# Optimization experiments

Hardware: AMD Instinct MI355X
Metric: run time of the kernel (lower is better)

## Reference

```python
import jax, jax.numpy as jnp
import numpy as np

B, N, L = 32, 1024, 128
K, D_E, H = 3, 16, 4


def setup_inputs() -> dict:
    key = jax.random.key(0)
    ks = jax.random.split(key, 7)
    return {
        "x": jax.random.normal(ks[0], (B, N, L), jnp.float32),
        # mild scaling on embeddings/projections keeps softmax logits in a sane range
        "psi_emb": jax.random.normal(ks[1], (N, D_E), jnp.float32) * 0.3,
        "psi": jnp.float32(1.0),
        "W_q": jax.random.normal(ks[2], (D_E, H, D_E), jnp.float32) * 0.2,
        "W_k": jax.random.normal(ks[3], (D_E, H, D_E), jnp.float32) * 0.2,
        "attn_alpha": jnp.float32(0.5),
        "F_w": jax.random.normal(ks[4], (H, D_E, K + 1, L), jnp.float32) * 0.1,
        "f_b": jax.random.normal(ks[5], (H, D_E), jnp.float32),
        "head_mix": jnp.ones((H,), jnp.float32),
    }


def reference(x, psi_emb, psi, W_q, W_k, attn_alpha, F_w, f_b, head_mix):
    # x: (B, N, L)
    n = x.shape[1]
    # --- gaussian adjacency: softmax over columns of exp(-psi * ||psi_i - psi_j||^2)
    diff = psi_emb[:, None, :] - psi_emb[None, :, :]          # (N, N, d_e)
    dist2 = jnp.sum(diff * diff, axis=-1)                     # (N, N)
    A_base = jax.nn.softmax(jnp.exp(-psi * dist2), axis=1)    # (N, N)
    # --- per-head attention adjacency
    Q = jnp.einsum('nd,dhm->nhm', psi_emb, W_q)               # (N, H, d_e)
    Kt = jnp.einsum('nd,dhm->nhm', psi_emb, W_k)              # (N, H, d_e)
    scale = 1.0 / jnp.sqrt(jnp.asarray(Q.shape[-1], x.dtype))
    A_attn = jax.nn.softmax(
        jnp.einsum('nhd,mhd->hnm', Q, Kt) * scale, axis=-1)   # (H, N, N)
    # --- sigmoid blend (all heads at once)
    alpha = jax.nn.sigmoid(attn_alpha)
    A_eff = alpha * A_base[None] + (1.0 - alpha) * A_attn     # (H, N, N)
    # --- Chebyshev recursion: T0 = I, T1 = A, Tk = 2 A T_{k-1} - T_{k-2}
    I = jnp.broadcast_to(jnp.eye(n, dtype=x.dtype), A_eff.shape)
    supports = [I, A_eff]
    for _ in range(2, K + 1):
        supports.append(2.0 * jnp.einsum('hnm,hml->hnl', A_eff, supports[-1]) - supports[-2])
    S = jnp.stack(supports, axis=1)                           # (H, K+1, N, N)
    # --- per-node filters
    W_filter = jnp.einsum('nd,hdkl->hnkl', psi_emb, F_w)      # (H, N, K+1, L)
    b_filter = jnp.einsum('nd,hd->hn', psi_emb, f_b)          # (H, N)
    # --- graph conv + node-specific contraction
    x_g = jnp.einsum('hknm,bml->bhknl', S, x)                 # (B, H, K+1, N, L)
    out_h = jnp.einsum('bhknl,hnkl->bhn', x_g, W_filter) + b_filter[None]
    # --- head mixing
    mix_w = jax.nn.softmax(head_mix, axis=0)                  # (H,)
    return jnp.einsum('bhn,h->bn', out_h, mix_w)              # (B, N)
```

## Files before the change

### kernel.cpp

```cpp
#include <hip/hip_runtime.h>
#include <cstdint>

#define NN 1024
#define BB 32
#define LL 128
#define DE 16
#define HH 4
#define K1 4
#define BD 512
#define NS 524288

using bf16x8 = __attribute__((ext_vector_type(8))) short;
using f32x4  = __attribute__((ext_vector_type(4))) float;

__device__ inline unsigned short f2bf(float f) {
    unsigned u = __builtin_bit_cast(unsigned, f);
    u += 0x7FFFu + ((u >> 16) & 1u);
    return (unsigned short)(u >> 16);
}
__device__ inline float bf2f(unsigned short u) {
    return __builtin_bit_cast(float, (unsigned)u << 16);
}

struct LogitsSmem {
    float ejs[64][17];
    float eis[64][17];
    float kjs[64][64];
    float qis[4][64][17];
    float part[4][5][64];
    float wq[1024];
    float wk[1024];
};
struct XtSmem { float xs[64][128]; };

__global__ __launch_bounds__(256) void phase1(
    const float* __restrict__ psi_emb, const float* __restrict__ psi_p,
    const float* __restrict__ W_q, const float* __restrict__ W_k,
    const float* __restrict__ x, const float* __restrict__ F_w,
    short* __restrict__ bnt, short* __restrict__ ant, float* __restrict__ partials,
    short* __restrict__ xt, short* __restrict__ wtt, float* __restrict__ out)
{
    __shared__ __align__(16) char smem_raw[sizeof(LogitsSmem)];
    const int bid = blockIdx.x;
    const int tid = threadIdx.x;

    if (bid < 256) {
        LogitsSmem& S = *(LogitsSmem*)smem_raw;
        const int jb = bid & 15, ib = bid >> 4;
        const int i0 = ib * 64, j0 = jb * 64;
        {
            const int row = tid >> 2, dq = (tid & 3) * 4;
            const float4 vj = *(const float4*)(psi_emb + (j0 + row) * DE + dq);
            S.ejs[row][dq] = vj.x; S.ejs[row][dq + 1] = vj.y;
            S.ejs[row][dq + 2] = vj.z; S.ejs[row][dq + 3] = vj.w;
            const float4 vi = *(const float4*)(psi_emb + (i0 + row) * DE + dq);
            S.eis[row][dq] = vi.x; S.eis[row][dq + 1] = vi.y;
            S.eis[row][dq + 2] = vi.z; S.eis[row][dq + 3] = vi.w;
            *(float4*)&S.wq[tid * 4] = *(const float4*)(W_q + tid * 4);
            *(float4*)&S.wk[tid * 4] = *(const float4*)(W_k + tid * 4);
        }
        __syncthreads();
#pragma unroll
        for (int rep = 0; rep < 16; rep++) {
            const int idx = rep * 256 + tid;
            const int row = idx >> 6, hm = idx & 63;
            float qv = 0.f, kv = 0.f;
#pragma unroll
            for (int d = 0; d < DE; d++) {
                qv += S.eis[row][d] * S.wq[d * 64 + hm];
                kv += S.ejs[row][d] * S.wk[d * 64 + hm];
            }
            S.qis[hm >> 4][row][hm & 15] = qv;
            S.kjs[row][hm] = kv;
        }
        __syncthreads();

        const int i = tid & 63, jg = tid >> 6;
        const float psi = psi_p[0];
        float er[DE];
#pragma unroll
        for (int d = 0; d < DE; d++) er[d] = S.eis[i][d];

        float sb = 0.f, sa[HH] = {0.f, 0.f, 0.f, 0.f};
#pragma unroll
        for (int g = 0; g < 2; g++) {
            unsigned short bw[8];
#pragma unroll
            for (int r = 0; r < 8; r++) {
                const int j = jg * 16 + g * 8 + r;
                float d2 = 0.f;
#pragma unroll
                for (int d = 0; d < DE; d++) { const float t = er[d] - S.ejs[j][d]; d2 += t * t; }
                const float bn = __expf(__expf(-psi * d2));
                sb += bn;
                bw[r] = f2bf(bn);
            }
            uint4 pk;
            pk.x = bw[0] | ((unsigned)bw[1] << 16);
            pk.y = bw[2] | ((unsigned)bw[3] << 16);
            pk.z = bw[4] | ((unsigned)bw[5] << 16);
            pk.w = bw[6] | ((unsigned)bw[7] << 16);
            const size_t toff = (size_t)((j0 + jg * 16 + g * 8) >> 3) * 8192 + (size_t)(i0 + i) * 8;
            *(uint4*)(bnt + toff) = pk;
        }
#pragma unroll
        for (int h = 0; h < HH; h++) {
            float qr[DE];
#pragma unroll
            for (int m = 0; m < DE; m++) qr[m] = S.qis[h][i][m];
#pragma unroll
            for (int g = 0; g < 2; g++) {
                unsigned short aw[8];
#pragma unroll
                for (int r = 0; r < 8; r++) {
                    const int j = jg * 16 + g * 8 + r;
                    float dot = 0.f;
#pragma unroll
                    for (int m = 0; m < DE; m++) dot += qr[m] * S.kjs[j][h * DE + m];
                    const float an = __expf(dot * 0.25f);
                    sa[h] += an;
                    aw[r] = f2bf(an);
                }
                uint4 pk;
                pk.x = aw[0] | ((unsigned)aw[1] << 16);
                pk.y = aw[2] | ((unsigned)aw[3] << 16);
                pk.z = aw[4] | ((unsigned)aw[5] << 16);
                pk.w = aw[6] | ((unsigned)aw[7] << 16);
                const size_t toff = (size_t)((j0 + jg * 16 + g * 8) >> 3) * 8192 + (size_t)(i0 + i) * 8;
                *(uint4*)(ant + (size_t)h * 1048576 + toff) = pk;
            }
        }
        S.part[jg][0][i] = sb;
#pragma unroll
        for (int h = 0; h < HH; h++) S.part[jg][1 + h][i] = sa[h];
        __syncthreads();
        if (tid < 64) {
#pragma unroll
            for (int s = 0; s < 5; s++) {
                const float v = S.part[0][s][tid] + S.part[1][s][tid] +
                                S.part[2][s][tid] + S.part[3][s][tid];
                partials[(size_t)jb * 5120 + (size_t)s * 1024 + i0 + tid] = v;
            }
        }
    } else if (bid < 768) {
        XtSmem& X = *(XtSmem*)smem_raw;
        const int idx = bid - 256;
        const int m0 = (idx & 15) * 64;
        const int b  = idx >> 4;
        for (int i = tid; i < 2048; i += 256) {
            const int row = i >> 5, lq = i & 31;
            *(float4*)&X.xs[row][lq * 4] =
                *(const float4*)(x + ((size_t)(b * NN + m0 + row)) * LL + lq * 4);
        }
        __syncthreads();
        for (int j = tid; j < 1024; j += 256) {
            const int m = j & 63, lc = j >> 6;
            const float* s = &X.xs[m][lc * 8];
            uint4 pk;
            pk.x = f2bf(s[0]) | ((unsigned)f2bf(s[1]) << 16);
            pk.y = f2bf(s[2]) | ((unsigned)f2bf(s[3]) << 16);
            pk.z = f2bf(s[4]) | ((unsigned)f2bf(s[5]) << 16);
            pk.w = f2bf(s[6]) | ((unsigned)f2bf(s[7]) << 16);
            *(uint4*)(xt + (size_t)b * 131072 + (size_t)lc * 8192 + (size_t)(m0 + m) * 8) = pk;
        }
    } else if (bid < 784) {
        const int j = (bid - 768) * 256 + tid;
        const int lc = j >> 8, c = j & 255;
        const int h = c >> 6, k = (c >> 4) & 3, d = c & 15;
        const float* s = F_w + (size_t)((h * DE + d) * K1 + k) * LL + lc * 8;
        uint4 pk;
        pk.x = f2bf(s[0]) | ((unsigned)f2bf(s[1]) << 16);
        pk.y = f2bf(s[2]) | ((unsigned)f2bf(s[3]) << 16);
        pk.z = f2bf(s[4]) | ((unsigned)f2bf(s[5]) << 16);
        pk.w = f2bf(s[6]) | ((unsigned)f2bf(s[7]) << 16);
        *(uint4*)(wtt + (size_t)lc * 2048 + (size_t)c * 8) = pk;
    } else {
        const int idx = (bid - 784) * 256 + tid;
        const float4 z = {0.f, 0.f, 0.f, 0.f};
        *(float4*)(out + (size_t)idx * 8) = z;
        *(float4*)(out + (size_t)idx * 8 + 4) = z;
    }
}

__global__ __launch_bounds__(256) void phase2(
    const short* __restrict__ xt, const short* __restrict__ wtt,
    short* __restrict__ Gt,
    const short* __restrict__ bnt, const short* __restrict__ ant,
    const float* __restrict__ partials, const float* __restrict__ alpha_p,
    short* __restrict__ At)
{
    const int bid = blockIdx.x;
    const int tid = threadIdx.x;
    __shared__ float sums_l[5][64];

    if (bid < 1024) {
        const int cb = bid & 3;
        const int m0 = ((bid >> 2) & 15) * 64;
        const int bp = bid >> 6;
        const int wave = tid >> 6, lane = tid & 63;
        const int b  = bp * 2 + (wave >> 1);
        const int wc = wave & 1;
        const int q = lane >> 4, m16 = lane & 15;
        const short* xb = xt + (size_t)b * 131072;

        f32x4 acc[4][2];
#pragma unroll
        for (int mi = 0; mi < 4; mi++)
#pragma unroll
            for (int ni = 0; ni < 2; ni++) acc[mi][ni] = (f32x4){0.f, 0.f, 0.f, 0.f};

#pragma unroll
        for (int ks = 0; ks < 4; ks++) {
            const int kc = ks * 4 + q;
            bf16x8 a[4], bb[2];
#pragma unroll
            for (int mi = 0; mi < 4; mi++)
                a[mi] = *(const bf16x8*)(xb + (size_t)kc * 8192 + (size_t)(m0 + mi * 16 + m16) * 8);
#pragma unroll
            for (int ni = 0; ni < 2; ni++)
                bb[ni] = *(const bf16x8*)(wtt + (size_t)kc * 2048 +
                                          (size_t)(cb * 64 + wc * 32 + ni * 16 + m16) * 8);
#pragma unroll
            for (int mi = 0; mi < 4; mi++)
#pragma unroll
                for (int ni = 0; ni < 2; ni++)
                    acc[mi][ni] = __builtin_amdgcn_mfma_f32_16x16x32_bf16(a[mi], bb[ni], acc[mi][ni], 0, 0, 0);
        }

#pragma unroll
        for (int ni = 0; ni < 2; ni++) {
            const int cc = cb * 64 + wc * 32 + ni * 16 + m16;
            const int kk = (cc >> 4) & 3, hh = cc >> 6;
            const int col512 = b * 16 + (cc & 15);
            short* gdst = Gt + (size_t)(kk * 4 + hh) * 524288;
#pragma unroll
            for (int mi = 0; mi < 4; mi++) {
                const int row0 = m0 + mi * 16 + q * 4;
                ushort4 pk;
                pk.x = f2bf(acc[mi][ni][0]); pk.y = f2bf(acc[mi][ni][1]);
                pk.z = f2bf(acc[mi][ni][2]); pk.w = f2bf(acc[mi][ni][3]);
                *(ushort4*)(gdst + ((size_t)(row0 >> 3) * 512 + col512) * 8 + (row0 & 7)) = pk;
            }
        }
    } else {
        const int idx = bid - 1024;
        const int jb = idx & 15, ib = idx >> 4;
        const int i0 = ib * 64, j0 = jb * 64;
        const int lane = tid & 63, w = tid >> 6;
        {
            float acc = 0.f;
#pragma unroll
            for (int jb2 = 0; jb2 < 16; jb2++)
                acc += partials[(size_t)jb2 * 5120 + (size_t)w * 1024 + i0 + lane];
            sums_l[w][lane] = acc;
            if (w == 0) {
                float a4 = 0.f;
#pragma unroll
                for (int jb2 = 0; jb2 < 16; jb2++)
                    a4 += partials[(size_t)jb2 * 5120 + 4 * 1024 + i0 + lane];
                sums_l[4][lane] = a4;
            }
        }
        __syncthreads();
        const int i = lane, jg = w;
        const float alpha = 1.f / (1.f + __expf(-alpha_p[0]));
        const float ibs = alpha / sums_l[0][i];
        float ias[HH];
#pragma unroll
        for (int h = 0; h < HH; h++) ias[h] = (1.f - alpha) / sums_l[1 + h][i];

#pragma unroll
        for (int g = 0; g < 2; g++) {
            const size_t toff = (size_t)((j0 + jg * 16 + g * 8) >> 3) * 8192 + (size_t)(i0 + i) * 8;
            const uint4 bp = *(const uint4*)(bnt + toff);
            float bnv[8];
            bnv[0] = bf2f(bp.x & 0xFFFF); bnv[1] = bf2f(bp.x >> 16);
            bnv[2] = bf2f(bp.y & 0xFFFF); bnv[3] = bf2f(bp.y >> 16);
            bnv[4] = bf2f(bp.z & 0xFFFF); bnv[5] = bf2f(bp.z >> 16);
            bnv[6] = bf2f(bp.w & 0xFFFF); bnv[7] = bf2f(bp.w >> 16);
#pragma unroll
            for (int h = 0; h < HH; h++) {
                const uint4 ap = *(const uint4*)(ant + (size_t)h * 1048576 + toff);
                float av[8];
                av[0] = bf2f(ap.x & 0xFFFF); av[1] = bf2f(ap.x >> 16);
                av[2] = bf2f(ap.y & 0xFFFF); av[3] = bf2f(ap.y >> 16);
                av[4] = bf2f(ap.z & 0xFFFF); av[5] = bf2f(ap.z >> 16);
                av[6] = bf2f(ap.w & 0xFFFF); av[7] = bf2f(ap.w >> 16);
                unsigned short ow[8];
#pragma unroll
                for (int r = 0; r < 8; r++) ow[r] = f2bf(ibs * bnv[r] + ias[h] * av[r]);
                uint4 pk;
                pk.x = ow[0] | ((unsigned)ow[1] << 16);
                pk.y = ow[2] | ((unsigned)ow[3] << 16);
                pk.z = ow[4] | ((unsigned)ow[5] << 16);
                pk.w = ow[6] | ((unsigned)ow[7] << 16);
                *(uint4*)(At + (size_t)h * 1048576 + toff) = pk;
            }
        }
    }
}

__global__ __launch_bounds__(256) void gemm_mf(
    const short* __restrict__ At, const short* __restrict__ Bt,
    const short* __restrict__ Pt, const short* __restrict__ Qt,
    short* __restrict__ Ot, float scale, float pc, float qc)
{
    const int h = blockIdx.z;
    const short* Ah = At + (size_t)h * 1048576;
    const short* Bh = Bt + (size_t)h * 524288;
    const short* Ph = Pt + (size_t)h * 524288;
    const short* Qh = Qt + (size_t)h * 524288;
    short* Oh = Ot + (size_t)h * 524288;

    const int c0 = blockIdx.x * 64;
    const int r0 = blockIdx.y * 64;
    const int tid = threadIdx.x;
    const int wave = tid >> 6, lane = tid & 63;
    const int q = lane >> 4, m16 = lane & 15;
    const int wr = wave >> 1, wc = wave & 1;

    __shared__ __align__(16) short As[2][2048];
    __shared__ __align__(16) short Bs[2][2048];

    {
        uint4 ra = *(const uint4*)(Ah + ((size_t)wave * 1024 + r0 + lane) * 8);
        uint4 rb = *(const uint4*)(Bh + ((size_t)wave * 512 + c0 + lane) * 8);
        *(uint4*)&As[0][wave * 512 + lane * 8] = ra;
        *(uint4*)&Bs[0][wave * 512 + lane * 8] = rb;
    }
    __syncthreads();

    f32x4 acc[2][2];
#pragma unroll
    for (int mi = 0; mi < 2; mi++)
#pragma unroll
        for (int ni = 0; ni < 2; ni++) acc[mi][ni] = (f32x4){0.f, 0.f, 0.f, 0.f};

    int buf = 0;
    for (int k0 = 32; k0 <= 1024; k0 += 32) {
        uint4 na, nb;
        const bool more = (k0 < 1024);
        if (more) {
            na = *(const uint4*)(Ah + (((size_t)(k0 >> 3) + wave) * 1024 + r0 + lane) * 8);
            nb = *(const uint4*)(Bh + (((size_t)(k0 >> 3) + wave) * 512 + c0 + lane) * 8);
        }
        bf16x8 af0 = *(const bf16x8*)&As[buf][q * 512 + (wr * 32 + m16) * 8];
        bf16x8 af1 = *(const bf16x8*)&As[buf][q * 512 + (wr * 32 + 16 + m16) * 8];
        bf16x8 bf0 = *(const bf16x8*)&Bs[buf][q * 512 + (wc * 32 + m16) * 8];
        bf16x8 bf1 = *(const bf16x8*)&Bs[buf][q * 512 + (wc * 32 + 16 + m16) * 8];
        acc[0][0] = __builtin_amdgcn_mfma_f32_16x16x32_bf16(af0, bf0, acc[0][0], 0, 0, 0);
        acc[0][1] = __builtin_amdgcn_mfma_f32_16x16x32_bf16(af0, bf1, acc[0][1], 0, 0, 0);
        acc[1][0] = __builtin_amdgcn_mfma_f32_16x16x32_bf16(af1, bf0, acc[1][0], 0, 0, 0);
        acc[1][1] = __builtin_amdgcn_mfma_f32_16x16x32_bf16(af1, bf1, acc[1][1], 0, 0, 0);
        if (more) {
            const int nx = buf ^ 1;
            *(uint4*)&As[nx][wave * 512 + lane * 8] = na;
            *(uint4*)&Bs[nx][wave * 512 + lane * 8] = nb;
            __syncthreads();
            buf = nx;
        }
    }

#pragma unroll
    for (int mi = 0; mi < 2; mi++) {
        const int row0 = r0 + wr * 32 + mi * 16 + q * 4;
#pragma unroll
        for (int ni = 0; ni < 2; ni++) {
            const int cc = c0 + wc * 32 + ni * 16 + m16;
            const size_t off = ((size_t)(row0 >> 3) * 512 + cc) * 8 + (row0 & 7);
            const ushort4 pv = *(const ushort4*)(Ph + off);
            float v[4];
            v[0] = scale * acc[mi][ni][0] + pc * bf2f(pv.x);
            v[1] = scale * acc[mi][ni][1] + pc * bf2f(pv.y);
            v[2] = scale * acc[mi][ni][2] + pc * bf2f(pv.z);
            v[3] = scale * acc[mi][ni][3] + pc * bf2f(pv.w);
            if (qc != 0.f) {
                const ushort4 qv = *(const ushort4*)(Qh + off);
                v[0] += qc * bf2f(qv.x); v[1] += qc * bf2f(qv.y);
                v[2] += qc * bf2f(qv.z); v[3] += qc * bf2f(qv.w);
            }
            ushort4 pk;
            pk.x = f2bf(v[0]); pk.y = f2bf(v[1]); pk.z = f2bf(v[2]); pk.w = f2bf(v[3]);
            *(ushort4*)(Oh + off) = pk;
        }
    }
}

__global__ __launch_bounds__(256) void gemm3_out(
    const short* __restrict__ At, const short* __restrict__ Bt,
    const short* __restrict__ Pt, const short* __restrict__ Qt,
    const float* __restrict__ psi_emb, const float* __restrict__ f_b,
    const float* __restrict__ head_mix, float* __restrict__ out)
{
    const int h = blockIdx.z;
    const short* Ah = At + (size_t)h * 1048576;
    const short* Bh = Bt + (size_t)h * 524288;
    const short* Ph = Pt + (size_t)h * 524288;
    const short* Qh = Qt + (size_t)h * 524288;

    const int c0 = blockIdx.x * 64;
    const int r0 = blockIdx.y * 64;
    const int tid = threadIdx.x;
    const int wave = tid >> 6, lane = tid & 63;
    const int q = lane >> 4, m16 = lane & 15;
    const int wr = wave >> 1, wc = wave & 1;

    __shared__ __align__(16) short As[2][2048];
    __shared__ __align__(16) short Bs[2][2048];
    __shared__ float es[64][17];

    {
        uint4 ra = *(const uint4*)(Ah + ((size_t)wave * 1024 + r0 + lane) * 8);
        uint4 rb = *(const uint4*)(Bh + ((size_t)wave * 512 + c0 + lane) * 8);
        *(uint4*)&As[0][wave * 512 + lane * 8] = ra;
        *(uint4*)&Bs[0][wave * 512 + lane * 8] = rb;
        const int row = tid >> 2, dq = (tid & 3) * 4;
        const float4 ev = *(const float4*)(psi_emb + (size_t)(r0 + row) * DE + dq);
        es[row][dq] = ev.x; es[row][dq + 1] = ev.y;
        es[row][dq + 2] = ev.z; es[row][dq + 3] = ev.w;
    }
    __syncthreads();

    f32x4 acc[2][2];
#pragma unroll
    for (int mi = 0; mi < 2; mi++)
#pragma unroll
        for (int ni = 0; ni < 2; ni++) acc[mi][ni] = (f32x4){0.f, 0.f, 0.f, 0.f};

    int buf = 0;
    for (int k0 = 32; k0 <= 1024; k0 += 32) {
        uint4 na, nb;
        const bool more = (k0 < 1024);
        if (more) {
            na = *(const uint4*)(Ah + (((size_t)(k0 >> 3) + wave) * 1024 + r0 + lane) * 8);
            nb = *(const uint4*)(Bh + (((size_t)(k0 >> 3) + wave) * 512 + c0 + lane) * 8);
        }
        bf16x8 af0 = *(const bf16x8*)&As[buf][q * 512 + (wr * 32 + m16) * 8];
        bf16x8 af1 = *(const bf16x8*)&As[buf][q * 512 + (wr * 32 + 16 + m16) * 8];
        bf16x8 bf0 = *(const bf16x8*)&Bs[buf][q * 512 + (wc * 32 + m16) * 8];
        bf16x8 bf1 = *(const bf16x8*)&Bs[buf][q * 512 + (wc * 32 + 16 + m16) * 8];
        acc[0][0] = __builtin_amdgcn_mfma_f32_16x16x32_bf16(af0, bf0, acc[0][0], 0, 0, 0);
        acc[0][1] = __builtin_amdgcn_mfma_f32_16x16x32_bf16(af0, bf1, acc[0][1], 0, 0, 0);
        acc[1][0] = __builtin_amdgcn_mfma_f32_16x16x32_bf16(af1, bf0, acc[1][0], 0, 0, 0);
        acc[1][1] = __builtin_amdgcn_mfma_f32_16x16x32_bf16(af1, bf1, acc[1][1], 0, 0, 0);
        if (more) {
            const int nx = buf ^ 1;
            *(uint4*)&As[nx][wave * 512 + lane * 8] = na;
            *(uint4*)&Bs[nx][wave * 512 + lane * 8] = nb;
            __syncthreads();
            buf = nx;
        }
    }

    const float hm0 = head_mix[0], hm1 = head_mix[1], hm2 = head_mix[2], hm3 = head_mix[3];
    const float mx = fmaxf(fmaxf(hm0, hm1), fmaxf(hm2, hm3));
    const float w0 = expf(hm0 - mx), w1 = expf(hm1 - mx), w2 = expf(hm2 - mx), w3 = expf(hm3 - mx);
    const float isum = 1.f / (w0 + w1 + w2 + w3);
    const float mwh = (h == 0 ? w0 : h == 1 ? w1 : h == 2 ? w2 : w3) * isum;
    const float fb = f_b[h * DE + m16];

#pragma unroll
    for (int mi = 0; mi < 2; mi++) {
        const int rloc0 = wr * 32 + mi * 16 + q * 4;
        const int row0 = r0 + rloc0;
#pragma unroll
        for (int ni = 0; ni < 2; ni++) {
            const int cc = c0 + wc * 32 + ni * 16 + m16;
            const int b = cc >> 4;
            const size_t off = ((size_t)(row0 >> 3) * 512 + cc) * 8 + (row0 & 7);
            const ushort4 pv = *(const ushort4*)(Ph + off);
            const ushort4 qv = *(const ushort4*)(Qh + off);
            float v[4];
            v[0] = acc[mi][ni][0] + bf2f(pv.x) - bf2f(qv.x);
            v[1] = acc[mi][ni][1] + bf2f(pv.y) - bf2f(qv.y);
            v[2] = acc[mi][ni][2] + bf2f(pv.z) - bf2f(qv.z);
            v[3] = acc[mi][ni][3] + bf2f(pv.w) - bf2f(qv.w);
#pragma unroll
            for (int r = 0; r < 4; r++) {
                float w = es[rloc0 + r][m16] * (v[r] + fb);
                w += __shfl_xor(w, 1, 64);
                w += __shfl_xor(w, 2, 64);
                w += __shfl_xor(w, 4, 64);
                w += __shfl_xor(w, 8, 64);
                if (m16 == 0)
                    atomicAdd(out + (size_t)b * NN + (row0 + r), mwh * w);
            }
        }
    }
}

extern "C" void kernel_launch(void* const* d_in, const int* in_sizes, int n_in,
                              void* d_out, int out_size, void* d_ws, size_t ws_size,
                              hipStream_t stream)
{
    const float* x          = (const float*)d_in[0];
    const float* psi_emb    = (const float*)d_in[1];
    const float* psi        = (const float*)d_in[2];
    const float* W_q        = (const float*)d_in[3];
    const float* W_k        = (const float*)d_in[4];
    const float* attn_alpha = (const float*)d_in[5];
    const float* F_w        = (const float*)d_in[6];
    const float* f_b        = (const float*)d_in[7];
    const float* head_mix   = (const float*)d_in[8];
    float* out = (float*)d_out;

    short* At  = (short*)d_ws;
    short* xt  = At + 4194304;
    short* wtt = xt + 4194304;
    short* Gt  = wtt + 32768;
    short* b2t = Gt + 8388608;
    short* b1t = b2t + 2097152;
    short* bnt = b1t + 2097152;
    short* ant = bnt + 1048576;
    float* partials = (float*)(ant + 4194304);

    const size_t need_bytes =
        (size_t)(4194304 + 4194304 + 32768 + 8388608 + 2097152 + 2097152 + 1048576 + 4194304) * 2 +
        (size_t)81920 * 4;
    if (ws_size < need_bytes) return;

    phase1<<<800, 256, 0, stream>>>(psi_emb, psi, W_q, W_k, x, F_w,
                                    bnt, ant, partials, xt, wtt, out);
    phase2<<<1280, 256, 0, stream>>>(xt, wtt, Gt, bnt, ant, partials,
                                     attn_alpha, At);

    const dim3 gg(BD / 64, NN / 64, HH);
    gemm_mf<<<gg, 256, 0, stream>>>(At, Gt + 12 * (size_t)524288, Gt + 8 * (size_t)524288,
                                    Gt , b2t, 2.f, 1.f, 0.f);
    gemm_mf<<<gg, 256, 0, stream>>>(At, b2t, Gt + 4 * (size_t)524288,
                                    Gt + 12 * (size_t)524288, b1t, 2.f, 1.f, -1.f);
    gemm3_out<<<gg, 256, 0, stream>>>(At, b1t, Gt, b2t, psi_emb, f_b, head_mix, out);
}
```

Before: 155.9 us.

## Load MFMA fragments directly from global memory, dropping LDS double buffering

The two Chebyshev GEMM kernels no longer stage A and B tiles through double-buffered shared memory with a barrier every k-step. Each lane now reads its bf16x8 MFMA fragments straight from the pre-packed global layout, in an unrolled loop of 32 iterations. This removes LDS traffic and per-iteration __syncthreads. In exchange, waves sharing a tile row or column load the same data redundantly from global memory and rely on L1/L2 caching, and there is no explicit prefetch.

```diff
diff --git a/kernel.cpp b/kernel.cpp
--- a/kernel.cpp
+++ b/kernel.cpp
@@ -319,16 +319,8 @@
     const int q = lane >> 4, m16 = lane & 15;
     const int wr = wave >> 1, wc = wave & 1;
 
-    __shared__ __align__(16) short As[2][2048];
-    __shared__ __align__(16) short Bs[2][2048];
-
-    {
-        uint4 ra = *(const uint4*)(Ah + ((size_t)wave * 1024 + r0 + lane) * 8);
-        uint4 rb = *(const uint4*)(Bh + ((size_t)wave * 512 + c0 + lane) * 8);
-        *(uint4*)&As[0][wave * 512 + lane * 8] = ra;
-        *(uint4*)&Bs[0][wave * 512 + lane * 8] = rb;
-    }
-    __syncthreads();
+    const short* Ap = Ah + (size_t)q * 8192 + (size_t)(r0 + wr * 32 + m16) * 8;
+    const short* Bp = Bh + (size_t)q * 4096 + (size_t)(c0 + wc * 32 + m16) * 8;
 
     f32x4 acc[2][2];
 #pragma unroll
@@ -336,29 +328,16 @@
 #pragma unroll
         for (int ni = 0; ni < 2; ni++) acc[mi][ni] = (f32x4){0.f, 0.f, 0.f, 0.f};
 
-    int buf = 0;
-    for (int k0 = 32; k0 <= 1024; k0 += 32) {
-        uint4 na, nb;
-        const bool more = (k0 < 1024);
-        if (more) {
-            na = *(const uint4*)(Ah + (((size_t)(k0 >> 3) + wave) * 1024 + r0 + lane) * 8);
-            nb = *(const uint4*)(Bh + (((size_t)(k0 >> 3) + wave) * 512 + c0 + lane) * 8);
-        }
-        bf16x8 af0 = *(const bf16x8*)&As[buf][q * 512 + (wr * 32 + m16) * 8];
-        bf16x8 af1 = *(const bf16x8*)&As[buf][q * 512 + (wr * 32 + 16 + m16) * 8];
-        bf16x8 bf0 = *(const bf16x8*)&Bs[buf][q * 512 + (wc * 32 + m16) * 8];
-        bf16x8 bf1 = *(const bf16x8*)&Bs[buf][q * 512 + (wc * 32 + 16 + m16) * 8];
+#pragma unroll 8
+    for (int it = 0; it < 32; it++) {
+        const bf16x8 af0 = *(const bf16x8*)(Ap + (size_t)it * 32768);
+        const bf16x8 af1 = *(const bf16x8*)(Ap + (size_t)it * 32768 + 128);
+        const bf16x8 bf0 = *(const bf16x8*)(Bp + (size_t)it * 16384);
+        const bf16x8 bf1 = *(const bf16x8*)(Bp + (size_t)it * 16384 + 128);
         acc[0][0] = __builtin_amdgcn_mfma_f32_16x16x32_bf16(af0, bf0, acc[0][0], 0, 0, 0);
         acc[0][1] = __builtin_amdgcn_mfma_f32_16x16x32_bf16(af0, bf1, acc[0][1], 0, 0, 0);
         acc[1][0] = __builtin_amdgcn_mfma_f32_16x16x32_bf16(af1, bf0, acc[1][0], 0, 0, 0);
         acc[1][1] = __builtin_amdgcn_mfma_f32_16x16x32_bf16(af1, bf1, acc[1][1], 0, 0, 0);
-        if (more) {
-            const int nx = buf ^ 1;
-            *(uint4*)&As[nx][wave * 512 + lane * 8] = na;
-            *(uint4*)&Bs[nx][wave * 512 + lane * 8] = nb;
-            __syncthreads();
-            buf = nx;
-        }
     }
 
 #pragma unroll
@@ -405,15 +384,8 @@
     const int q = lane >> 4, m16 = lane & 15;
     const int wr = wave >> 1, wc = wave & 1;
 
-    __shared__ __align__(16) short As[2][2048];
-    __shared__ __align__(16) short Bs[2][2048];
     __shared__ float es[64][17];
-
     {
-        uint4 ra = *(const uint4*)(Ah + ((size_t)wave * 1024 + r0 + lane) * 8);
-        uint4 rb = *(const uint4*)(Bh + ((size_t)wave * 512 + c0 + lane) * 8);
-        *(uint4*)&As[0][wave * 512 + lane * 8] = ra;
-        *(uint4*)&Bs[0][wave * 512 + lane * 8] = rb;
         const int row = tid >> 2, dq = (tid & 3) * 4;
         const float4 ev = *(const float4*)(psi_emb + (size_t)(r0 + row) * DE + dq);
         es[row][dq] = ev.x; es[row][dq + 1] = ev.y;
@@ -421,35 +393,25 @@
     }
     __syncthreads();
 
+    const short* Ap = Ah + (size_t)q * 8192 + (size_t)(r0 + wr * 32 + m16) * 8;
+    const short* Bp = Bh + (size_t)q * 4096 + (size_t)(c0 + wc * 32 + m16) * 8;
+
     f32x4 acc[2][2];
 #pragma unroll
     for (int mi = 0; mi < 2; mi++)
 #pragma unroll
         for (int ni = 0; ni < 2; ni++) acc[mi][ni] = (f32x4){0.f, 0.f, 0.f, 0.f};
 
-    int buf = 0;
-    for (int k0 = 32; k0 <= 1024; k0 += 32) {
-        uint4 na, nb;
-        const bool more = (k0 < 1024);
-        if (more) {
-            na = *(const uint4*)(Ah + (((size_t)(k0 >> 3) + wave) * 1024 + r0 + lane) * 8);
-            nb = *(const uint4*)(Bh + (((size_t)(k0 >> 3) + wave) * 512 + c0 + lane) * 8);
-        }
-        bf16x8 af0 = *(const bf16x8*)&As[buf][q * 512 + (wr * 32 + m16) * 8];
-        bf16x8 af1 = *(const bf16x8*)&As[buf][q * 512 + (wr * 32 + 16 + m16) * 8];
-        bf16x8 bf0 = *(const bf16x8*)&Bs[buf][q * 512 + (wc * 32 + m16) * 8];
-        bf16x8 bf1 = *(const bf16x8*)&Bs[buf][q * 512 + (wc * 32 + 16 + m16) * 8];
+#pragma unroll 8
+    for (int it = 0; it < 32; it++) {
+        const bf16x8 af0 = *(const bf16x8*)(Ap + (size_t)it * 32768);
+        const bf16x8 af1 = *(const bf16x8*)(Ap + (size_t)it * 32768 + 128);
+        const bf16x8 bf0 = *(const bf16x8*)(Bp + (size_t)it * 16384);
+        const bf16x8 bf1 = *(const bf16x8*)(Bp + (size_t)it * 16384 + 128);
         acc[0][0] = __builtin_amdgcn_mfma_f32_16x16x32_bf16(af0, bf0, acc[0][0], 0, 0, 0);
         acc[0][1] = __builtin_amdgcn_mfma_f32_16x16x32_bf16(af0, bf1, acc[0][1], 0, 0, 0);
         acc[1][0] = __builtin_amdgcn_mfma_f32_16x16x32_bf16(af1, bf0, acc[1][0], 0, 0, 0);
         acc[1][1] = __builtin_amdgcn_mfma_f32_16x16x32_bf16(af1, bf1, acc[1][1], 0, 0, 0);
-        if (more) {
-            const int nx = buf ^ 1;
-            *(uint4*)&As[nx][wave * 512 + lane * 8] = na;
-            *(uint4*)&Bs[nx][wave * 512 + lane * 8] = nb;
-            __syncthreads();
-            buf = nx;
-        }
     }
 
     const float hm0 = head_mix[0], hm1 = head_mix[1], hm2 = head_mix[2], hm3 = head_mix[3];
```

Measured after the change: 151.8 us. 1.03x faster.
